# Performance work log

Hardware: AMD Instinct MI355X
Metric: run time of the kernel (lower is better)

Reference implementation:

```python
import jax, jax.numpy as jnp
import numpy as np

B, L = 64, 2048
V, E, G = 30, 128, 8          # n_tokens, embedding_size, n_globals
C, F, O = 64, 128, 30         # res_channels, f_channels, n_outputs
K, ND = 2, 9                  # kernel_size, n_dilations
GE = G * E                    # flattened global embedding dim


def causal_conv(x, w, b, dilation):
    # x: [B,Cin,L], w: [Cout,Cin,K] -> [B,Cout,L], causal via left padding
    pad = (w.shape[-1] - 1) * dilation
    out = jax.lax.conv_general_dilated(
        x, w, window_strides=(1,), padding=[(pad, 0)],
        rhs_dilation=(dilation,), dimension_numbers=("NCH", "OIH", "NCH"))
    return out + b[None, :, None]


def setup_inputs() -> dict:
    key = jax.random.key(0)
    ks = jax.random.split(key, 20)
    s = 0.05
    inp = {
        "input_tensor": jax.random.randint(ks[0], (B, L), 0, V),
        "global_input": jax.random.randint(ks[1], (B, G), 0, V),
        "emb_table": jax.random.normal(ks[2], (V, E), jnp.float32) * s,
        "w_causal": jax.random.normal(ks[3], (C, E, K), jnp.float32) * s,
        "b_causal": jnp.zeros((C,), jnp.float32),
        "w_f": jax.random.normal(ks[4], (ND, C, C, K), jnp.float32) * s,
        "b_f": jnp.zeros((ND, C), jnp.float32),
        "w_g": jax.random.normal(ks[5], (ND, C, C, K), jnp.float32) * s,
        "b_g": jnp.zeros((ND, C), jnp.float32),
        "wl_f": jax.random.normal(ks[6], (ND, C, GE), jnp.float32) * s,
        "bl_f": jnp.zeros((ND, C), jnp.float32),
        "wl_g": jax.random.normal(ks[7], (ND, C, GE), jnp.float32) * s,
        "bl_g": jnp.zeros((ND, C), jnp.float32),
        "w_res": jax.random.normal(ks[8], (ND, C, C), jnp.float32) * s,
        "b_res": jnp.zeros((ND, C), jnp.float32),
        "w_fin1": jax.random.normal(ks[9], (F, C), jnp.float32) * s,
        "b_fin1": jnp.zeros((F,), jnp.float32),
        "w_fin2": jax.random.normal(ks[10], (O, F), jnp.float32) * s,
        "b_fin2": jnp.zeros((O,), jnp.float32),
    }
    return inp


def reference(input_tensor, global_input, emb_table, w_causal, b_causal,
              w_f, b_f, w_g, b_g, wl_f, bl_f, wl_g, bl_g,
              w_res, b_res, w_fin1, b_fin1, w_fin2, b_fin2):
    # padding_idx=0: row 0 is zero and receives no gradient
    table = emb_table.at[0].set(0.0)
    emb = table[input_tensor]                     # [B,L,E]
    emb_g = table[global_input].reshape(B, GE)    # [B,G*E]
    x = jnp.transpose(emb, (0, 2, 1))             # [B,E,L]
    res = causal_conv(x, w_causal, b_causal, 1)   # [B,C,L]
    skips = jnp.zeros_like(res)
    for i in range(ND):
        d = 2 ** (i + 1)
        h_f = emb_g @ wl_f[i].T + bl_f[i]         # [B,C]
        h_g = emb_g @ wl_g[i].T + bl_g[i]
        x_f = causal_conv(res, w_f[i], b_f[i], d) + h_f[:, :, None]
        x_g = causal_conv(res, w_g[i], b_g[i], d) + h_g[:, :, None]
        z = jnp.tanh(x_f) * jax.nn.sigmoid(x_g)   # gated activation
        skip = jnp.einsum("oc,bcl->bol", w_res[i], z) + b_res[i][None, :, None]
        res = res + skip
        skips = skips + skip
    out = jax.nn.relu(skips)
    out = jnp.einsum("fc,bcl->bfl", w_fin1, out) + b_fin1[None, :, None]
    out = jax.nn.relu(out)
    out = jnp.einsum("of,bfl->bol", w_fin2, out) + b_fin2[None, :, None]
    return out
```

## Files before the change

kernel.cpp:

```cpp
#include <hip/hip_runtime.h>
#include <stdint.h>

#define Bz 64
#define Lz 2048
#define Vz 30
#define Ez 128
#define Gz 8
#define Cz 64
#define Fz 128
#define Oz 30
#define NDz 9

typedef __attribute__((ext_vector_type(8))) short short8;
typedef _Float16 half8 __attribute__((ext_vector_type(8)));
typedef __fp16 fp16x2 __attribute__((ext_vector_type(2)));
typedef __attribute__((ext_vector_type(4))) float floatx4;

#define MFMA16B __builtin_amdgcn_mfma_f32_16x16x32_bf16
#define MFMA16H __builtin_amdgcn_mfma_f32_16x16x32_f16

__device__ __forceinline__ uint16_t f2bf(float f) {
    uint32_t u = __float_as_uint(f);
    u += 0x7fffu + ((u >> 16) & 1u);
    return (uint16_t)(u >> 16);
}
__device__ __forceinline__ uint16_t f2h(float f) {
    return __builtin_bit_cast(uint16_t, (_Float16)f);
}
__device__ __forceinline__ uint32_t pk2h(float lo, float hi) {
    fp16x2 h = __builtin_amdgcn_cvt_pkrtz(lo, hi);
    return __builtin_bit_cast(uint32_t, h);
}
__device__ __forceinline__ uint32_t pkadd(uint32_t oldbits, float a, float b) {
    fp16x2 h = __builtin_bit_cast(fp16x2, oldbits) + __builtin_amdgcn_cvt_pkrtz(a, b);
    return __builtin_bit_cast(uint32_t, h);
}
__device__ __forceinline__ float h2f(uint32_t u16bits) {
    return (float)__builtin_bit_cast(_Float16, (uint16_t)u16bits);
}
__device__ __forceinline__ float gatefn(float f, float g) {
    float a = __expf(2.f * f);
    float b = __expf(-g);
    float ap1 = a + 1.f;
    return (a - 1.f) * __builtin_amdgcn_rcpf(fmaf(ap1, b, ap1));
}

#define N_WB   (NDz * 128 * 128)
#define N_WR   (NDz * 64 * 64)
#define N_W1   (Fz * Cz)
#define N_W2   (32 * Fz)
#define N_PROJ (Vz * Cz)
#define N_WLB  (NDz * 128 * 1024)
#define N_EMB  (Bz * 1024)
#define N_BIAS (NDz * 128)

__global__ void pack_k(const float* __restrict__ w_f, const float* __restrict__ w_g,
                       const float* __restrict__ w_res, const float* __restrict__ w_fin1,
                       const float* __restrict__ w_fin2, const float* __restrict__ w_causal,
                       const float* __restrict__ table, const int* __restrict__ gin,
                       const float* __restrict__ wl_f, const float* __restrict__ wl_g,
                       const float* __restrict__ b_f, const float* __restrict__ b_g,
                       const float* __restrict__ bl_f, const float* __restrict__ bl_g,
                       uint16_t* __restrict__ WB, uint16_t* __restrict__ WrB,
                       uint16_t* __restrict__ W1B, uint16_t* __restrict__ W2B,
                       float* __restrict__ proj0, float* __restrict__ proj1,
                       uint16_t* __restrict__ WLB, uint16_t* __restrict__ embG,
                       float* __restrict__ biasrow) {
    int tid = blockIdx.x * 256 + threadIdx.x;
    if (tid < N_WB) {
        int i = tid >> 14, rem = tid & 16383, ch = rem >> 7, k = rem & 127;
        int kin = k & 63, tap = (k < 64) ? 1 : 0;
        float v = (ch < 64) ? w_f[((i * Cz + ch) * Cz + kin) * 2 + tap]
                            : w_g[((i * Cz + (ch - 64)) * Cz + kin) * 2 + tap];
        WB[tid] = f2h(v);
        return;
    }
    tid -= N_WB;
    if (tid < N_WR) { WrB[tid] = f2h(w_res[tid]); return; }
    tid -= N_WR;
    if (tid < N_W1) { W1B[tid] = f2h(w_fin1[tid]); return; }
    tid -= N_W1;
    if (tid < N_W2) {
        int o = tid >> 7, f = tid & 127;
        W2B[tid] = f2h(o < Oz ? w_fin2[o * Fz + f] : 0.f);
        return;
    }
    tid -= N_W2;
    if (tid < N_PROJ) {
        int v = tid >> 6, c = tid & 63;
        float s0 = 0.f, s1 = 0.f;
        if (v != 0) {
            for (int e = 0; e < Ez; e++) {
                float tv = table[v * Ez + e];
                s0 += w_causal[(c * Ez + e) * 2 + 0] * tv;
                s1 += w_causal[(c * Ez + e) * 2 + 1] * tv;
            }
        }
        proj0[tid] = s0; proj1[tid] = s1;
        return;
    }
    tid -= N_PROJ;
    if (tid < N_WLB) {
        int row = tid >> 10, j = tid & 1023;
        int i = row >> 7, rem = row & 127, fg = rem >> 6, c = rem & 63;
        const float* wl = fg ? wl_g : wl_f;
        WLB[tid] = f2bf(wl[((size_t)(i * Cz + c)) * 1024 + j]);
        return;
    }
    tid -= N_WLB;
    if (tid < N_EMB) {
        int b = tid >> 10, j = tid & 1023;
        int g = j >> 7, e = j & 127;
        int v = gin[b * Gz + g];
        embG[tid] = f2bf(v ? table[v * Ez + e] : 0.f);
        return;
    }
    tid -= N_EMB;
    if (tid < N_BIAS) {
        int i = tid >> 7, rem = tid & 127, fg = rem >> 6, c = rem & 63;
        biasrow[tid] = (fg ? b_g : b_f)[i * Cz + c] + (fg ? bl_g : bl_f)[i * Cz + c];
    }
}

__global__ __launch_bounds__(256) void hgemm_k(
    const uint16_t* __restrict__ WLB, const uint16_t* __restrict__ embG,
    const float* __restrict__ biasrow, float* __restrict__ hhT) {
    int tx = threadIdx.x, lane = tx & 63, wave = tx >> 6;
    int nl = lane & 15, quad = lane >> 4;
    int row0 = blockIdx.x * 64 + wave * 16;
    floatx4 acc[4];
    float bv[4];
#pragma unroll
    for (int r = 0; r < 4; r++) bv[r] = biasrow[row0 + quad * 4 + r];
#pragma unroll
    for (int nt = 0; nt < 4; nt++)
#pragma unroll
        for (int r = 0; r < 4; r++) acc[nt][r] = bv[r];
    const uint16_t* ap = WLB + (size_t)(row0 + nl) * 1024 + quad * 8;
#pragma unroll 4
    for (int ks = 0; ks < 32; ks++) {
        short8 a = *(const short8*)(ap + ks * 32);
#pragma unroll
        for (int nt = 0; nt < 4; nt++) {
            short8 bb = *(const short8*)(embG + (size_t)(nt * 16 + nl) * 1024 + ks * 32 + quad * 8);
            acc[nt] = MFMA16B(a, bb, acc[nt], 0, 0, 0);
        }
    }
#pragma unroll
    for (int nt = 0; nt < 4; nt++)
#pragma unroll
        for (int r = 0; r < 4; r++)
            hhT[(size_t)(row0 + quad * 4 + r) * 64 + nt * 16 + nl] = acc[nt][r];
}

__global__ __launch_bounds__(256) void init_k(
    const int* __restrict__ tok, const float* __restrict__ b_causal,
    const float* __restrict__ proj0, const float* __restrict__ proj1,
    uint16_t* __restrict__ res) {
    int tx = threadIdx.x;
    int q = tx & 15, tl = tx >> 4;
    int b = blockIdx.y;
    int t = blockIdx.x * 16 + tl;
    int v1 = tok[b * Lz + t];
    int v0 = (t > 0) ? tok[b * Lz + t - 1] : 0;
    float4 p1 = ((const float4*)(proj1 + v1 * Cz))[q];
    float4 p0 = ((const float4*)(proj0 + v0 * Cz))[q];
    float4 bc = ((const float4*)b_causal)[q];
    float rx = p1.x + p0.x + bc.x, ry = p1.y + p0.y + bc.y;
    float rz = p1.z + p0.z + bc.z, rw = p1.w + p0.w + bc.w;
    *(uint2*)(res + ((size_t)(b * Lz + t)) * Cz + q * 4) =
        make_uint2(pk2h(rx, ry), pk2h(rz, rw));
}

__global__ __launch_bounds__(256, 2) void fused_k(
    const uint16_t* __restrict__ rin, uint16_t* __restrict__ rout,
    const uint16_t* __restrict__ WB, const uint16_t* __restrict__ WrB,
    const float* __restrict__ hhT, const float* __restrict__ b_res) {
    __shared__ __align__(16) uint16_t R[256 * 72];
    __shared__ __align__(16) uint16_t Zb[256 * 72];
    int tx = threadIdx.x;
    int lane = tx & 63, wave = tx >> 6;
    int nl = lane & 15, quad = lane >> 4;
    int b = blockIdx.y, t0 = blockIdx.x * 128;
    const uint16_t* rb16 = rin + ((size_t)b * Lz) * Cz;

    if (t0 != 0) {
        const uint16_t* src = rb16 + (size_t)(t0 - 128) * Cz;
#pragma unroll
        for (int it = 0; it < 8; it++) {
            int id = it * 256 + tx, row = id >> 3, c8 = id & 7;
            uint4 v = *(const uint4*)(src + (size_t)row * Cz + c8 * 8);
            *(uint4*)(R + row * 72 + c8 * 8) = v;
        }
    } else {
#pragma unroll
        for (int it = 0; it < 8; it++) {
            int id = it * 256 + tx, row = id >> 3, c8 = id & 7;
            int t = row - 128;
            uint4 v = make_uint4(0u, 0u, 0u, 0u);
            if (t >= 0) v = *(const uint4*)(rb16 + (size_t)t * Cz + c8 * 8);
            *(uint4*)(R + row * 72 + c8 * 8) = v;
        }
    }
    floatx4 ss[8];
#pragma unroll
    for (int j = 0; j < 8; j++)
#pragma unroll
        for (int r = 0; r < 4; r++) ss[j][r] = 0.f;
    __syncthreads();

    const int chq = wave * 16 + quad * 4;
    const int NT0[6] = {0, 0, 1, 2, 4, 8};

#pragma unroll
    for (int l = 0; l < 6; l++) {
        const int d = 2 << l;
        const int nt0 = NT0[l];
        const uint16_t* wf = WB + l * 16384 + (wave * 16 + nl) * 128 + quad * 8;
        half8 AF[4], AG[4];
#pragma unroll
        for (int ks = 0; ks < 4; ks++) {
            AF[ks] = *(const half8*)(wf + ks * 32);
            AG[ks] = *(const half8*)(wf + 64 * 128 + ks * 32);
        }
        const uint16_t* wr = WrB + l * 4096 + (wave * 16 + nl) * 64 + quad * 8;
        half8 AR0 = *(const half8*)(wr);
        half8 AR1 = *(const half8*)(wr + 32);
        float hfv[4], hgv[4], brv[4];
        const float* hp = hhT + ((size_t)(l * 128 + wave * 16 + quad * 4)) * 64 + b;
#pragma unroll
        for (int r = 0; r < 4; r++) { hfv[r] = hp[r * 64]; hgv[r] = hp[4096 + r * 64]; }
        const float* brp = b_res + l * Cz + wave * 16 + quad * 4;
#pragma unroll
        for (int r = 0; r < 4; r++) brv[r] = brp[r];

#pragma unroll
        for (int nt = 0; nt < 16; nt++) {
            if (nt < nt0) continue;
            int rowa = nt * 16 + nl;
            int rowb = rowa - d;
            if (nt * 16 < d) rowb = rowb < 0 ? 0 : rowb;
            const uint16_t* ra = R + rowa * 72 + quad * 8;
            const uint16_t* rb = R + rowb * 72 + quad * 8;
            half8 b0 = *(const half8*)(ra);
            half8 b1 = *(const half8*)(ra + 32);
            half8 b2 = *(const half8*)(rb);
            half8 b3 = *(const half8*)(rb + 32);
            floatx4 aF, aG;
#pragma unroll
            for (int r = 0; r < 4; r++) { aF[r] = hfv[r]; aG[r] = hgv[r]; }
            aF = MFMA16H(AF[0], b0, aF, 0, 0, 0); aG = MFMA16H(AG[0], b0, aG, 0, 0, 0);
            aF = MFMA16H(AF[1], b1, aF, 0, 0, 0); aG = MFMA16H(AG[1], b1, aG, 0, 0, 0);
            aF = MFMA16H(AF[2], b2, aF, 0, 0, 0); aG = MFMA16H(AG[2], b2, aG, 0, 0, 0);
            aF = MFMA16H(AF[3], b3, aF, 0, 0, 0); aG = MFMA16H(AG[3], b3, aG, 0, 0, 0);
            float z0 = gatefn(aF[0], aG[0]);
            float z1 = gatefn(aF[1], aG[1]);
            float z2 = gatefn(aF[2], aG[2]);
            float z3 = gatefn(aF[3], aG[3]);
            *(uint2*)(Zb + rowa * 72 + chq) = make_uint2(pk2h(z0, z1), pk2h(z2, z3));
        }
        __syncthreads();

        if (t0 != 0) {
#pragma unroll
            for (int nt = 0; nt < 16; nt++) {
                if (nt < nt0) continue;
                int pos = nt * 16 + nl;
                const uint16_t* zp = Zb + pos * 72 + quad * 8;
                floatx4 a2;
#pragma unroll
                for (int r = 0; r < 4; r++) a2[r] = brv[r];
                a2 = MFMA16H(AR0, *(const half8*)zp, a2, 0, 0, 0);
                a2 = MFMA16H(AR1, *(const half8*)(zp + 32), a2, 0, 0, 0);
                uint16_t* rp = R + pos * 72 + chq;
                uint2 oldp = *(uint2*)rp;
                *(uint2*)rp = make_uint2(pkadd(oldp.x, a2[0], a2[1]),
                                         pkadd(oldp.y, a2[2], a2[3]));
                if (nt >= 8) {
#pragma unroll
                    for (int r = 0; r < 4; r++) ss[nt - 8][r] += a2[r];
                }
            }
        } else {
#pragma unroll
            for (int nt = 0; nt < 16; nt++) {
                if (nt < nt0) continue;
                int pos = nt * 16 + nl;
                const uint16_t* zp = Zb + pos * 72 + quad * 8;
                floatx4 a2;
#pragma unroll
                for (int r = 0; r < 4; r++) a2[r] = brv[r];
                a2 = MFMA16H(AR0, *(const half8*)zp, a2, 0, 0, 0);
                a2 = MFMA16H(AR1, *(const half8*)(zp + 32), a2, 0, 0, 0);
                bool ok = (pos >= 128);
                uint16_t* rp = R + pos * 72 + chq;
                uint2 oldp = *(uint2*)rp;
                uint32_t ux = ok ? pkadd(oldp.x, a2[0], a2[1]) : 0u;
                uint32_t uy = ok ? pkadd(oldp.y, a2[2], a2[3]) : 0u;
                *(uint2*)rp = make_uint2(ux, uy);
                if (nt >= 8) {
#pragma unroll
                    for (int r = 0; r < 4; r++) ss[nt - 8][r] += a2[r];
                }
            }
        }
        __syncthreads();
    }

    uint16_t* ro = rout + ((size_t)b * Lz) * Cz;
#pragma unroll
    for (int j = 0; j < 8; j++) {
        size_t off = (size_t)(t0 + j * 16 + nl) * Cz + chq;
        uint2 rv = *(const uint2*)(rb16 + off);
        *(uint2*)(ro + off) = make_uint2(pkadd(rv.x, ss[j][0], ss[j][1]),
                                         pkadd(rv.y, ss[j][2], ss[j][3]));
    }
}

__global__ __launch_bounds__(256, 4) void layer_k(
    const uint16_t* __restrict__ rin, uint16_t* __restrict__ rout,
    const uint16_t* __restrict__ WBl, const uint16_t* __restrict__ WrBl,
    const float* __restrict__ hhT, const float* __restrict__ b_res,
    int i, int d) {
    __shared__ __align__(16) uint16_t X[64 * 136];
    __shared__ __align__(16) uint16_t Z[64 * 72];
    int tx = threadIdx.x;
    int lane = tx & 63, wave = tx >> 6;
    int nl = lane & 15, quad = lane >> 4;
    int b = blockIdx.y, t0 = blockIdx.x * 64;
    const uint16_t* rb16 = rin + ((size_t)b * Lz) * Cz;

#pragma unroll
    for (int it = 0; it < 2; it++) {
        int id = it * 256 + tx, row = id >> 3, c8 = id & 7;
        uint4 v = *(const uint4*)(rb16 + (size_t)(t0 + row) * Cz + c8 * 8);
        *(uint4*)(X + row * 136 + c8 * 8) = v;
    }
#pragma unroll
    for (int it = 0; it < 2; it++) {
        int id = it * 256 + tx, row = id >> 3, c8 = id & 7;
        int tb = t0 + row - d;
        uint4 v = make_uint4(0u, 0u, 0u, 0u);
        if (tb >= 0) v = *(const uint4*)(rb16 + (size_t)tb * Cz + c8 * 8);
        *(uint4*)(X + row * 136 + 64 + c8 * 8) = v;
    }

    half8 AF[4], AG[4], AR[2];
    {
        const uint16_t* wf = WBl + (wave * 16 + nl) * 128 + quad * 8;
#pragma unroll
        for (int ks = 0; ks < 4; ks++) {
            AF[ks] = *(const half8*)(wf + ks * 32);
            AG[ks] = *(const half8*)(wf + 64 * 128 + ks * 32);
        }
        const uint16_t* wr = WrBl + (wave * 16 + nl) * 64 + quad * 8;
#pragma unroll
        for (int ks = 0; ks < 2; ks++) AR[ks] = *(const half8*)(wr + ks * 32);
    }
    float hfv[4], hgv[4], brv[4];
    {
        const float* hp = hhT + ((size_t)(i * 128 + wave * 16 + quad * 4)) * 64 + b;
#pragma unroll
        for (int r = 0; r < 4; r++) {
            hfv[r] = hp[r * 64];
            hgv[r] = hp[4096 + r * 64];
        }
        const float* brp = b_res + i * Cz + wave * 16 + quad * 4;
#pragma unroll
        for (int r = 0; r < 4; r++) brv[r] = brp[r];
    }
    __syncthreads();

    floatx4 accF[4], accG[4];
#pragma unroll
    for (int nt = 0; nt < 4; nt++)
#pragma unroll
        for (int r = 0; r < 4; r++) { accF[nt][r] = hfv[r]; accG[nt][r] = hgv[r]; }
#pragma unroll
    for (int nt = 0; nt < 4; nt++) {
        const uint16_t* xp = X + (nt * 16 + nl) * 136 + quad * 8;
#pragma unroll
        for (int ks = 0; ks < 4; ks++) {
            half8 bf = *(const half8*)(xp + ks * 32);
            accF[nt] = MFMA16H(AF[ks], bf, accF[nt], 0, 0, 0);
            accG[nt] = MFMA16H(AG[ks], bf, accG[nt], 0, 0, 0);
        }
    }

    int chq = wave * 16 + quad * 4;
#pragma unroll
    for (int nt = 0; nt < 4; nt++) {
        int pos = nt * 16 + nl;
        float z0 = gatefn(accF[nt][0], accG[nt][0]);
        float z1 = gatefn(accF[nt][1], accG[nt][1]);
        float z2 = gatefn(accF[nt][2], accG[nt][2]);
        float z3 = gatefn(accF[nt][3], accG[nt][3]);
        *(uint2*)(Z + pos * 72 + chq) = make_uint2(pk2h(z0, z1), pk2h(z2, z3));
    }
    __syncthreads();

    floatx4 acc2[4];
#pragma unroll
    for (int nt = 0; nt < 4; nt++)
#pragma unroll
        for (int r = 0; r < 4; r++) acc2[nt][r] = brv[r];
#pragma unroll
    for (int nt = 0; nt < 4; nt++) {
        const uint16_t* zp = Z + (nt * 16 + nl) * 72 + quad * 8;
        acc2[nt] = MFMA16H(AR[0], *(const half8*)zp, acc2[nt], 0, 0, 0);
        acc2[nt] = MFMA16H(AR[1], *(const half8*)(zp + 32), acc2[nt], 0, 0, 0);
    }

    uint16_t* ro = rout + ((size_t)b * Lz) * Cz;
#pragma unroll
    for (int nt = 0; nt < 4; nt++) {
        size_t off = (size_t)(t0 + nt * 16 + nl) * Cz + chq;
        uint2 rv = *(const uint2*)(rb16 + off);
        *(uint2*)(ro + off) = make_uint2(pkadd(rv.x, acc2[nt][0], acc2[nt][1]),
                                         pkadd(rv.y, acc2[nt][2], acc2[nt][3]));
    }
}

__global__ __launch_bounds__(256, 3) void final_k(
    const uint16_t* __restrict__ res0, const uint16_t* __restrict__ resF,
    const uint16_t* __restrict__ W1B, const uint16_t* __restrict__ W2B,
    const float* __restrict__ b_fin1, const float* __restrict__ b_fin2,
    float* __restrict__ out) {
    __shared__ __align__(16) uint16_t S[128 * 72];
    __shared__ __align__(16) uint16_t Mi[128 * 136];
    int tx = threadIdx.x;
    int lane = tx & 63, wave = tx >> 6;
    int nl = lane & 15, quad = lane >> 4;
    int b = blockIdx.y, t0 = blockIdx.x * 128;
    const uint16_t* r0 = res0 + ((size_t)b * Lz) * Cz;
    const uint16_t* rF = resF + ((size_t)b * Lz) * Cz;

    half8 A1[2][2], A2[2][4];
#pragma unroll
    for (int mt = 0; mt < 2; mt++) {
        const uint16_t* w1 = W1B + (wave * 32 + mt * 16 + nl) * 64 + quad * 8;
#pragma unroll
        for (int ks = 0; ks < 2; ks++) A1[mt][ks] = *(const half8*)(w1 + ks * 32);
        const uint16_t* w2 = W2B + (mt * 16 + nl) * 128 + quad * 8;
#pragma unroll
        for (int ks = 0; ks < 4; ks++) A2[mt][ks] = *(const half8*)(w2 + ks * 32);
    }
#pragma unroll
    for (int it = 0; it < 4; it++) {
        int id = it * 256 + tx, row = id >> 3, c8 = id & 7;
        uint4 fv = *(const uint4*)(rF + (size_t)(t0 + row) * Cz + c8 * 8);
        uint4 ov = *(const uint4*)(r0 + (size_t)(t0 + row) * Cz + c8 * 8);
        float s0 = fmaxf(h2f(fv.x) - h2f(ov.x), 0.f);
        float s1 = fmaxf(h2f(fv.x >> 16) - h2f(ov.x >> 16), 0.f);
        float s2 = fmaxf(h2f(fv.y) - h2f(ov.y), 0.f);
        float s3 = fmaxf(h2f(fv.y >> 16) - h2f(ov.y >> 16), 0.f);
        float s4 = fmaxf(h2f(fv.z) - h2f(ov.z), 0.f);
        float s5 = fmaxf(h2f(fv.z >> 16) - h2f(ov.z >> 16), 0.f);
        float s6 = fmaxf(h2f(fv.w) - h2f(ov.w), 0.f);
        float s7 = fmaxf(h2f(fv.w >> 16) - h2f(ov.w >> 16), 0.f);
        *(uint4*)(S + row * 72 + c8 * 8) =
            make_uint4(pk2h(s0, s1), pk2h(s2, s3), pk2h(s4, s5), pk2h(s6, s7));
    }
    __syncthreads();

    floatx4 accM[2][8];
    float b1v[2][4];
#pragma unroll
    for (int mt = 0; mt < 2; mt++)
#pragma unroll
        for (int r = 0; r < 4; r++) b1v[mt][r] = b_fin1[wave * 32 + mt * 16 + quad * 4 + r];
#pragma unroll
    for (int mt = 0; mt < 2; mt++)
#pragma unroll
        for (int nt = 0; nt < 8; nt++)
#pragma unroll
            for (int r = 0; r < 4; r++) accM[mt][nt][r] = b1v[mt][r];
#pragma unroll
    for (int nt = 0; nt < 8; nt++) {
        const uint16_t* sp = S + (nt * 16 + nl) * 72 + quad * 8;
#pragma unroll
        for (int ks = 0; ks < 2; ks++) {
            half8 s = *(const half8*)(sp + ks * 32);
            accM[0][nt] = MFMA16H(A1[0][ks], s, accM[0][nt], 0, 0, 0);
            accM[1][nt] = MFMA16H(A1[1][ks], s, accM[1][nt], 0, 0, 0);
        }
    }
#pragma unroll
    for (int mt = 0; mt < 2; mt++)
#pragma unroll
        for (int nt = 0; nt < 8; nt++) {
            int pos = nt * 16 + nl;
            int fq = wave * 32 + mt * 16 + quad * 4;
            float m0 = fmaxf(accM[mt][nt][0], 0.f), m1 = fmaxf(accM[mt][nt][1], 0.f);
            float m2 = fmaxf(accM[mt][nt][2], 0.f), m3 = fmaxf(accM[mt][nt][3], 0.f);
            *(uint2*)(Mi + pos * 136 + fq) = make_uint2(pk2h(m0, m1), pk2h(m2, m3));
        }
    __syncthreads();

    floatx4 accO[2][2];
#pragma unroll
    for (int mt = 0; mt < 2; mt++)
#pragma unroll
        for (int r = 0; r < 4; r++) {
            int o = mt * 16 + quad * 4 + r;
            float bo = (o < Oz) ? b_fin2[o] : 0.f;
            accO[mt][0][r] = bo; accO[mt][1][r] = bo;
        }
#pragma unroll
    for (int ntl = 0; ntl < 2; ntl++) {
        int nt = wave * 2 + ntl;
        const uint16_t* mp = Mi + (nt * 16 + nl) * 136 + quad * 8;
#pragma unroll
        for (int ks = 0; ks < 4; ks++) {
            half8 m = *(const half8*)(mp + ks * 32);
            accO[0][ntl] = MFMA16H(A2[0][ks], m, accO[0][ntl], 0, 0, 0);
            accO[1][ntl] = MFMA16H(A2[1][ks], m, accO[1][ntl], 0, 0, 0);
        }
    }
#pragma unroll
    for (int mt = 0; mt < 2; mt++)
#pragma unroll
        for (int ntl = 0; ntl < 2; ntl++)
#pragma unroll
            for (int r = 0; r < 4; r++) {
                int o = mt * 16 + quad * 4 + r;
                if (o < Oz)
                    out[((size_t)b * Oz + o) * Lz + t0 + (wave * 2 + ntl) * 16 + nl] =
                        accO[mt][ntl][r];
            }
}

extern "C" void kernel_launch(void* const* d_in, const int* in_sizes, int n_in,
                              void* d_out, int out_size, void* d_ws, size_t ws_size,
                              hipStream_t stream) {
    const int*   tok      = (const int*)d_in[0];
    const int*   gin      = (const int*)d_in[1];
    const float* table    = (const float*)d_in[2];
    const float* w_causal = (const float*)d_in[3];
    const float* b_causal = (const float*)d_in[4];
    const float* w_f      = (const float*)d_in[5];
    const float* b_f      = (const float*)d_in[6];
    const float* w_g      = (const float*)d_in[7];
    const float* b_g      = (const float*)d_in[8];
    const float* wl_f     = (const float*)d_in[9];
    const float* bl_f     = (const float*)d_in[10];
    const float* wl_g     = (const float*)d_in[11];
    const float* bl_g     = (const float*)d_in[12];
    const float* w_res    = (const float*)d_in[13];
    const float* b_res    = (const float*)d_in[14];
    const float* w_fin1   = (const float*)d_in[15];
    const float* b_fin1   = (const float*)d_in[16];
    const float* w_fin2   = (const float*)d_in[17];
    const float* b_fin2   = (const float*)d_in[18];
    float* out = (float*)d_out;

    const size_t NRES = (size_t)Bz * Lz * Cz;
    uint16_t* u16 = (uint16_t*)d_ws;
    uint16_t* resA = u16;
    uint16_t* resB = resA + NRES;
    uint16_t* resC = resB + NRES;
    uint16_t* WB   = resC + NRES;
    uint16_t* WrB  = WB + N_WB;
    uint16_t* W1B  = WrB + N_WR;
    uint16_t* W2B  = W1B + N_W1;
    uint16_t* WLB  = W2B + N_W2;
    uint16_t* embG = WLB + N_WLB;
    float* hhT     = (float*)(embG + N_EMB);
    float* proj0   = hhT + 73728;
    float* proj1   = proj0 + N_PROJ;
    float* biasrow = proj1 + N_PROJ;

    int npack = N_WB + N_WR + N_W1 + N_W2 + N_PROJ + N_WLB + N_EMB + N_BIAS;
    pack_k<<<(npack + 255) / 256, 256, 0, stream>>>(
        w_f, w_g, w_res, w_fin1, w_fin2, w_causal, table, gin,
        wl_f, wl_g, b_f, b_g, bl_f, bl_g,
        WB, WrB, W1B, W2B, proj0, proj1, WLB, embG, biasrow);
    hgemm_k<<<18, 256, 0, stream>>>(WLB, embG, biasrow, hhT);
    init_k<<<dim3(Lz / 16, Bz), 256, 0, stream>>>(tok, b_causal, proj0, proj1, resA);

    fused_k<<<dim3(Lz / 128, Bz), 256, 0, stream>>>(resA, resB, WB, WrB, hhT, b_res);
    layer_k<<<dim3(Lz / 64, Bz), 256, 0, stream>>>(
        resB, resC, WB + (size_t)6 * 16384, WrB + (size_t)6 * 4096, hhT, b_res, 6, 128);
    layer_k<<<dim3(Lz / 64, Bz), 256, 0, stream>>>(
        resC, resB, WB + (size_t)7 * 16384, WrB + (size_t)7 * 4096, hhT, b_res, 7, 256);
    layer_k<<<dim3(Lz / 64, Bz), 256, 0, stream>>>(
        resB, resC, WB + (size_t)8 * 16384, WrB + (size_t)8 * 4096, hhT, b_res, 8, 512);
    final_k<<<dim3(Lz / 128, Bz), 256, 0, stream>>>(resA, resC, W1B, W2B,
                                                    b_fin1, b_fin2, out);
}
```

Before: 292.9 us.

## Fold exp scaling into weights, shrink Z buffer with swizzle, skip halo work

The ln2 and sign factors of the gate exponentials are folded into the packed conv weights, global-projection weights and biases, so the gate can call the native exp2 without extra multiplies. In the fused multi-layer kernel the Z staging buffer is halved and XOR-swizzled to avoid LDS bank conflicts. The main tile is processed first, and halo rows are recomputed only for early layers whose outputs are still needed and only for non-first tiles. Smaller shared memory lets the launch bounds rise to 3 and 6 blocks per SM, at the cost of more register pressure, one extra barrier pair in early layers, and slightly different rounding from the prescaled fp16/bf16 weights.

```diff
diff --git a/kernel.cpp b/kernel.cpp
--- a/kernel.cpp
+++ b/kernel.cpp
@@ -11,6 +11,9 @@
 #define Oz 30
 #define NDz 9
 
+#define TWOLOG2E 2.8853900817779268f
+#define NLOG2E  -1.4426950408889634f
+
 typedef __attribute__((ext_vector_type(8))) short short8;
 typedef _Float16 half8 __attribute__((ext_vector_type(8)));
 typedef __fp16 fp16x2 __attribute__((ext_vector_type(2)));
@@ -38,9 +41,16 @@
 __device__ __forceinline__ float h2f(uint32_t u16bits) {
     return (float)__builtin_bit_cast(_Float16, (uint16_t)u16bits);
 }
-__device__ __forceinline__ float gatefn(float f, float g) {
-    float a = __expf(2.f * f);
-    float b = __expf(-g);
+__device__ __forceinline__ float fexp2(float x) {
+#if __has_builtin(__builtin_amdgcn_exp2f)
+    return __builtin_amdgcn_exp2f(x);
+#else
+    float r; asm("v_exp_f32 %0, %1" : "=v"(r) : "v"(x)); return r;
+#endif
+}
+__device__ __forceinline__ float gatefn(float fl, float gl) {
+    float a = fexp2(fl);
+    float b = fexp2(gl);
     float ap1 = a + 1.f;
     return (a - 1.f) * __builtin_amdgcn_rcpf(fmaf(ap1, b, ap1));
 }
@@ -70,8 +80,8 @@
     if (tid < N_WB) {
         int i = tid >> 14, rem = tid & 16383, ch = rem >> 7, k = rem & 127;
         int kin = k & 63, tap = (k < 64) ? 1 : 0;
-        float v = (ch < 64) ? w_f[((i * Cz + ch) * Cz + kin) * 2 + tap]
-                            : w_g[((i * Cz + (ch - 64)) * Cz + kin) * 2 + tap];
+        float v = (ch < 64) ? w_f[((i * Cz + ch) * Cz + kin) * 2 + tap] * TWOLOG2E
+                            : w_g[((i * Cz + (ch - 64)) * Cz + kin) * 2 + tap] * NLOG2E;
         WB[tid] = f2h(v);
         return;
     }
@@ -104,7 +114,8 @@
         int row = tid >> 10, j = tid & 1023;
         int i = row >> 7, rem = row & 127, fg = rem >> 6, c = rem & 63;
         const float* wl = fg ? wl_g : wl_f;
-        WLB[tid] = f2bf(wl[((size_t)(i * Cz + c)) * 1024 + j]);
+        float sc = fg ? NLOG2E : TWOLOG2E;
+        WLB[tid] = f2bf(wl[((size_t)(i * Cz + c)) * 1024 + j] * sc);
         return;
     }
     tid -= N_WLB;
@@ -118,7 +129,8 @@
     tid -= N_EMB;
     if (tid < N_BIAS) {
         int i = tid >> 7, rem = tid & 127, fg = rem >> 6, c = rem & 63;
-        biasrow[tid] = (fg ? b_g : b_f)[i * Cz + c] + (fg ? bl_g : bl_f)[i * Cz + c];
+        float bsum = (fg ? b_g : b_f)[i * Cz + c] + (fg ? bl_g : bl_f)[i * Cz + c];
+        biasrow[tid] = bsum * (fg ? NLOG2E : TWOLOG2E);
     }
 }
 
@@ -172,12 +184,12 @@
         make_uint2(pk2h(rx, ry), pk2h(rz, rw));
 }
 
-__global__ __launch_bounds__(256, 2) void fused_k(
+__global__ __launch_bounds__(256, 3) void fused_k(
     const uint16_t* __restrict__ rin, uint16_t* __restrict__ rout,
     const uint16_t* __restrict__ WB, const uint16_t* __restrict__ WrB,
     const float* __restrict__ hhT, const float* __restrict__ b_res) {
     __shared__ __align__(16) uint16_t R[256 * 72];
-    __shared__ __align__(16) uint16_t Zb[256 * 72];
+    __shared__ __align__(16) uint16_t Zb[128 * 64];
     int tx = threadIdx.x;
     int lane = tx & 63, wave = tx >> 6;
     int nl = lane & 15, quad = lane >> 4;
@@ -210,6 +222,10 @@
     __syncthreads();
 
     const int chq = wave * 16 + quad * 4;
+    const int zmask = (nl & 7) << 3;
+    const int zwr  = chq ^ zmask;
+    const int zrd0 = (quad * 8) ^ zmask;
+    const int zrd1 = (quad * 8 + 32) ^ zmask;
     const int NT0[6] = {0, 0, 1, 2, 4, 8};
 
 #pragma unroll
@@ -235,11 +251,9 @@
         for (int r = 0; r < 4; r++) brv[r] = brp[r];
 
 #pragma unroll
-        for (int nt = 0; nt < 16; nt++) {
-            if (nt < nt0) continue;
+        for (int nt = 8; nt < 16; nt++) {
             int rowa = nt * 16 + nl;
             int rowb = rowa - d;
-            if (nt * 16 < d) rowb = rowb < 0 ? 0 : rowb;
             const uint16_t* ra = R + rowa * 72 + quad * 8;
             const uint16_t* rb = R + rowb * 72 + quad * 8;
             half8 b0 = *(const half8*)(ra);
@@ -257,54 +271,72 @@
             float z1 = gatefn(aF[1], aG[1]);
             float z2 = gatefn(aF[2], aG[2]);
             float z3 = gatefn(aF[3], aG[3]);
-            *(uint2*)(Zb + rowa * 72 + chq) = make_uint2(pk2h(z0, z1), pk2h(z2, z3));
+            *(uint2*)(Zb + (rowa - 128) * 64 + zwr) = make_uint2(pk2h(z0, z1), pk2h(z2, z3));
         }
         __syncthreads();
 
-        if (t0 != 0) {
-#pragma unroll
-            for (int nt = 0; nt < 16; nt++) {
+#pragma unroll
+        for (int nt = 8; nt < 16; nt++) {
+            int pos = nt * 16 + nl;
+            const uint16_t* zb0 = Zb + (pos - 128) * 64;
+            floatx4 a2;
+#pragma unroll
+            for (int r = 0; r < 4; r++) a2[r] = brv[r];
+            a2 = MFMA16H(AR0, *(const half8*)(zb0 + zrd0), a2, 0, 0, 0);
+            a2 = MFMA16H(AR1, *(const half8*)(zb0 + zrd1), a2, 0, 0, 0);
+            uint16_t* rp = R + pos * 72 + chq;
+            uint2 oldp = *(uint2*)rp;
+            *(uint2*)rp = make_uint2(pkadd(oldp.x, a2[0], a2[1]),
+                                     pkadd(oldp.y, a2[2], a2[3]));
+#pragma unroll
+            for (int r = 0; r < 4; r++) ss[nt - 8][r] += a2[r];
+        }
+        __syncthreads();
+
+        if (l < 5 && t0 != 0) {
+#pragma unroll
+            for (int nt = 0; nt < 8; nt++) {
+                if (nt < nt0) continue;
+                int rowa = nt * 16 + nl;
+                int rowb = rowa - d;
+                if (nt * 16 < d) rowb = rowb < 0 ? 0 : rowb;
+                const uint16_t* ra = R + rowa * 72 + quad * 8;
+                const uint16_t* rb = R + rowb * 72 + quad * 8;
+                half8 b0 = *(const half8*)(ra);
+                half8 b1 = *(const half8*)(ra + 32);
+                half8 b2 = *(const half8*)(rb);
+                half8 b3 = *(const half8*)(rb + 32);
+                floatx4 aF, aG;
+#pragma unroll
+                for (int r = 0; r < 4; r++) { aF[r] = hfv[r]; aG[r] = hgv[r]; }
+                aF = MFMA16H(AF[0], b0, aF, 0, 0, 0); aG = MFMA16H(AG[0], b0, aG, 0, 0, 0);
+                aF = MFMA16H(AF[1], b1, aF, 0, 0, 0); aG = MFMA16H(AG[1], b1, aG, 0, 0, 0);
+                aF = MFMA16H(AF[2], b2, aF, 0, 0, 0); aG = MFMA16H(AG[2], b2, aG, 0, 0, 0);
+                aF = MFMA16H(AF[3], b3, aF, 0, 0, 0); aG = MFMA16H(AG[3], b3, aG, 0, 0, 0);
+                float z0 = gatefn(aF[0], aG[0]);
+                float z1 = gatefn(aF[1], aG[1]);
+                float z2 = gatefn(aF[2], aG[2]);
+                float z3 = gatefn(aF[3], aG[3]);
+                *(uint2*)(Zb + rowa * 64 + zwr) = make_uint2(pk2h(z0, z1), pk2h(z2, z3));
+            }
+            __syncthreads();
+#pragma unroll
+            for (int nt = 0; nt < 8; nt++) {
                 if (nt < nt0) continue;
                 int pos = nt * 16 + nl;
-                const uint16_t* zp = Zb + pos * 72 + quad * 8;
+                const uint16_t* zb0 = Zb + pos * 64;
                 floatx4 a2;
 #pragma unroll
                 for (int r = 0; r < 4; r++) a2[r] = brv[r];
-                a2 = MFMA16H(AR0, *(const half8*)zp, a2, 0, 0, 0);
-                a2 = MFMA16H(AR1, *(const half8*)(zp + 32), a2, 0, 0, 0);
+                a2 = MFMA16H(AR0, *(const half8*)(zb0 + zrd0), a2, 0, 0, 0);
+                a2 = MFMA16H(AR1, *(const half8*)(zb0 + zrd1), a2, 0, 0, 0);
                 uint16_t* rp = R + pos * 72 + chq;
                 uint2 oldp = *(uint2*)rp;
                 *(uint2*)rp = make_uint2(pkadd(oldp.x, a2[0], a2[1]),
                                          pkadd(oldp.y, a2[2], a2[3]));
-                if (nt >= 8) {
-#pragma unroll
-                    for (int r = 0; r < 4; r++) ss[nt - 8][r] += a2[r];
-                }
             }
-        } else {
-#pragma unroll
-            for (int nt = 0; nt < 16; nt++) {
-                if (nt < nt0) continue;
-                int pos = nt * 16 + nl;
-                const uint16_t* zp = Zb + pos * 72 + quad * 8;
-                floatx4 a2;
-#pragma unroll
-                for (int r = 0; r < 4; r++) a2[r] = brv[r];
-                a2 = MFMA16H(AR0, *(const half8*)zp, a2, 0, 0, 0);
-                a2 = MFMA16H(AR1, *(const half8*)(zp + 32), a2, 0, 0, 0);
-                bool ok = (pos >= 128);
-                uint16_t* rp = R + pos * 72 + chq;
-                uint2 oldp = *(uint2*)rp;
-                uint32_t ux = ok ? pkadd(oldp.x, a2[0], a2[1]) : 0u;
-                uint32_t uy = ok ? pkadd(oldp.y, a2[2], a2[3]) : 0u;
-                *(uint2*)rp = make_uint2(ux, uy);
-                if (nt >= 8) {
-#pragma unroll
-                    for (int r = 0; r < 4; r++) ss[nt - 8][r] += a2[r];
-                }
-            }
-        }
-        __syncthreads();
+            __syncthreads();
+        }
     }
 
     uint16_t* ro = rout + ((size_t)b * Lz) * Cz;
@@ -317,7 +349,7 @@
     }
 }
 
-__global__ __launch_bounds__(256, 4) void layer_k(
+__global__ __launch_bounds__(256, 6) void layer_k(
     const uint16_t* __restrict__ rin, uint16_t* __restrict__ rout,
     const uint16_t* __restrict__ WBl, const uint16_t* __restrict__ WrBl,
     const float* __restrict__ hhT, const float* __restrict__ b_res,
```

Measured after the change: 369.5 us. +26.2%, slower.
